# Optimization experiments

Hardware: AMD Instinct MI355X
Metric: run time of the kernel (lower is better)

## Reference

```python
import jax, jax.numpy as jnp
import numpy as np

K = 30  # hardcoded top-k in take_top_k_dropout(x, 30, ...)


def _topk_channel_mask(x, k):
    # x: [B, C, H, W]; binary mask with 1 at the top-k |x| channels per pixel.
    B, C, H, W = x.shape
    xa = jnp.abs(x).reshape(B, C, H * W).transpose(0, 2, 1).reshape(B * H * W, C)
    _, idx = jax.lax.top_k(xa, k)  # [BHW, k]
    rows = jnp.arange(B * H * W)[:, None]
    mask = jnp.zeros((B * H * W, C), x.dtype).at[rows, idx].set(1.0)
    return mask.reshape(B, H * W, C).transpose(0, 2, 1).reshape(B, C, H, W)


def _saturation(z, phi, jump):
    # Saturation_activation_per_filter.forward
    l1 = (jnp.sum(jnp.abs(phi), axis=0) + 1e-12).reshape(1, -1, 1, 1)  # [1,C,1,1]
    r = z / l1
    r = 0.5 * (jnp.sign(r - jump) + jnp.sign(r + jump))
    return r * l1


def _conv_transpose(x, w, b, stride):
    # PyTorch ConvTranspose2d(padding=0): w is [in, out, kh, kw]
    k = w.shape[-1]
    wt = jnp.flip(w, (2, 3)).transpose(1, 0, 2, 3)  # -> [out, in, kh, kw]
    y = jax.lax.conv_general_dilated(
        x, wt, window_strides=(1, 1),
        padding=[(k - 1, k - 1), (k - 1, k - 1)],
        lhs_dilation=(stride, stride),
        dimension_numbers=('NCHW', 'OIHW', 'NCHW'))
    return y + b.reshape(1, -1, 1, 1)


def _take_middle(x):
    width = x.shape[-1]
    s = (width - 32) // 2
    return x[:, :, s:s + 32, s:s + 32]


def setup_inputs() -> dict:
    key = jax.random.key(0)
    ks = jax.random.split(key, 9)
    B, C, H, W, D = 128, 500, 16, 16, 192
    return {
        'x': jax.random.normal(ks[0], (B, C, H, W), jnp.float32),
        'phi': jax.random.normal(ks[1], (D, C), jnp.float32),
        'jump': jnp.float32(0.1),
        'w1': jax.random.normal(ks[2], (C, 300, 4, 4), jnp.float32) * 0.02,
        'b1': jax.random.normal(ks[3], (300,), jnp.float32) * 0.02,
        'w2': jax.random.normal(ks[4], (300, 100, 3, 3), jnp.float32) * 0.02,
        'b2': jax.random.normal(ks[5], (100,), jnp.float32) * 0.02,
        'w3': jax.random.normal(ks[6], (100, 3, 3, 3), jnp.float32) * 0.02,
        'b3': jax.random.normal(ks[7], (3,), jnp.float32) * 0.02,
    }


def reference(x, phi, jump, w1, b1, w2, b2, w3, b3):
    # eval mode: dropout(ones) == ones, no training rescalings
    out = x * _topk_channel_mask(x, K)
    out = _saturation(out, phi, jump)
    out = jax.nn.relu(_conv_transpose(out, w1, b1, 2))
    out = jax.nn.relu(_conv_transpose(out, w2, b2, 1))
    out = jax.nn.relu(_conv_transpose(out, w3, b3, 1))
    return _take_middle(out)
```

## Files before the change

### kernel.cpp

```cpp
#include <hip/hip_runtime.h>
#include <stdint.h>

#define B_   128
#define C_   500
#define H_   16
#define P_   256
#define D_   192
#define C1O  300
#define H1   34
#define P1   (H1*H1)
#define C2O  100
#define H2   36
#define P2   (H2*H2)
#define C3O  3
#define H3   38
#define P3   (H3*H3)
#define CROP 3
#define OW_  32
#define KTOP 30

#define NZQBLK (B_ * 4)
#define NB3BLK ((P3 + 3) / 4)

__device__ __forceinline__ float sgnf(float v){ return (v > 0.f) ? 1.f : ((v < 0.f) ? -1.f : 0.f); }

__device__ __forceinline__ int pat36(int i){
  if (i == 0) return 0;
  if (i == 1) return 1;
  if (i <= 33) return 2;
  if (i == 34) return 3;
  return 4;
}

__global__ void k_setup(const float* __restrict__ phi, const float* __restrict__ jumpp,
                        const float* __restrict__ w2, const float* __restrict__ b1,
                        const float* __restrict__ b2,
                        float* __restrict__ l1, float* __restrict__ thr,
                        float* __restrict__ tab, float4* __restrict__ zero_region){
  const int blk = blockIdx.x;
  const int t = threadIdx.x;

  if (blk >= 101){
    const int idx0 = (blk - 101) * 256 + t;
    const int nvec = (B_ * P1 + B_ * P2) / 16;
    float4 z = make_float4(0.f, 0.f, 0.f, 0.f);
    for (int i = idx0; i < nvec; i += 64 * 256) zero_region[i] = z;
    return;
  }

  if (blk == 100){
    float J = jumpp[0];
    for (int c = t; c < C_; c += 256){
      float s = 0.f;
      for (int d = 0; d < D_; ++d) s += fabsf(phi[d * C_ + c]);
      s += 1e-12f;
      l1[c] = s;
      thr[c] = J * s;
    }
    return;
  }

  __shared__ float S[9];
  if (t < 64){
    const int o = blk;
    float acc[9] = {0,0,0,0,0,0,0,0,0};
    for (int c = t; c < C1O; c += 64){
      float a1 = fmaxf(b1[c], 0.f);
      const float* w = w2 + (c * C2O + o) * 9;
#pragma unroll
      for (int tap = 0; tap < 9; ++tap) acc[tap] += w[tap] * a1;
    }
#pragma unroll
    for (int tap = 0; tap < 9; ++tap)
      for (int off = 32; off; off >>= 1) acc[tap] += __shfl_down(acc[tap], off);
    if (t == 0){
#pragma unroll
      for (int tap = 0; tap < 9; ++tap) S[tap] = acc[tap];
    }
  }
  __syncthreads();
  if (t < 25){
    const int lo[5] = {0,0,0,1,2}, hi[5] = {0,1,2,2,2};
    int pr = t / 5, pc = t % 5;
    float s = b2[blk];
    for (int kh = lo[pr]; kh <= hi[pr]; ++kh)
      for (int kw = lo[pc]; kw <= hi[pc]; ++kw) s += S[kh * 3 + kw];
    tab[blk * 25 + t] = s;
  }
}

__global__ void k_zq_b3(const float* __restrict__ x, const float* __restrict__ l1,
                        const float* __restrict__ thr, const float* __restrict__ jumpp,
                        const float* __restrict__ tab, const float* __restrict__ w3,
                        const float* __restrict__ b3,
                        signed char* __restrict__ zq, unsigned char* __restrict__ d0,
                        float* __restrict__ base3){
  if (blockIdx.x >= NZQBLK){
    const int wave = threadIdx.x >> 6, lane = threadIdx.x & 63;
    const int pix = (blockIdx.x - NZQBLK) * 4 + wave;
    if (pix >= P3) return;
    const int oh = pix / H3, ow = pix % H3;
    float acc[3] = {0, 0, 0};
    for (int c = lane; c < C2O; c += 64){
      const float* w = w3 + c * 27;
#pragma unroll
      for (int kh = 0; kh < 3; ++kh){
        int ih = oh - kh; if (ih < 0 || ih >= H2) continue;
        int prr = pat36(ih) * 5;
#pragma unroll
        for (int kw = 0; kw < 3; ++kw){
          int iw = ow - kw; if (iw < 0 || iw >= H2) continue;
          float a2 = fmaxf(tab[c * 25 + prr + pat36(iw)], 0.f);
#pragma unroll
          for (int o = 0; o < 3; ++o) acc[o] += w[o * 9 + kh * 3 + kw] * a2;
        }
      }
    }
#pragma unroll
    for (int o = 0; o < 3; ++o){
      for (int off = 32; off; off >>= 1) acc[o] += __shfl_down(acc[o], off);
    }
    if (lane == 0){
#pragma unroll
      for (int o = 0; o < 3; ++o) base3[o * P3 + pix] = acc[o] + b3[o];
    }
    return;
  }

  const int b = blockIdx.x >> 2;
  const int tile = (blockIdx.x & 3) * 64;
  const int t = threadIdx.x;
  const int q = t & 15, cg = t >> 4;

  __shared__ unsigned char um[256];
  __shared__ unsigned char pixf[64];
  __shared__ int s_any;
  if (t == 0) s_any = 0;

  unsigned m = 0;
  const int pbase = tile + 4 * q;
  for (int c = cg; c < C_; c += 16){
    float tc = thr[c];
    const float4 v = *(const float4*)(x + ((size_t)(b * C_ + c)) * P_ + pbase);
    if (fabsf(v.x) >= tc) m |= 1u;
    if (fabsf(v.y) >= tc) m |= 2u;
    if (fabsf(v.z) >= tc) m |= 4u;
    if (fabsf(v.w) >= tc) m |= 8u;
  }
  um[t] = (unsigned char)m;
  __syncthreads();
  if (t < 16){
    unsigned mm = 0;
#pragma unroll
    for (int g = 0; g < 16; ++g) mm |= um[g * 16 + t];
#pragma unroll
    for (int j = 0; j < 4; ++j){
      unsigned char f = (unsigned char)((mm >> j) & 1u);
      pixf[4 * t + j] = f;
      d0[b * P_ + tile + 4 * t + j] = f;
    }
    if (mm) s_any = 1;
  }
  __syncthreads();
  if (!s_any) return;

  __shared__ float sx[C_];
  __shared__ unsigned char rm[C_];
  __shared__ unsigned long long red[4];
  __shared__ int sel[KTOP];
  float J = jumpp[0];
  for (int pp = 0; pp < 64; ++pp){
    if (!pixf[pp]) continue;
    int px = tile + pp;
    for (int c = t; c < C_; c += 256){ sx[c] = x[(b * C_ + c) * P_ + px]; rm[c] = 0; }
    __syncthreads();
    for (int it = 0; it < KTOP; ++it){
      unsigned long long best = 0ULL;
      for (int c = t; c < C_; c += 256){
        if (!rm[c]){
          unsigned long long key =
            ((unsigned long long)__float_as_uint(fabsf(sx[c])) << 32) |
            (unsigned int)(C_ - 1 - c);
          if (key > best) best = key;
        }
      }
      for (int off = 32; off; off >>= 1){
        unsigned long long o2 = __shfl_down(best, off);
        if (o2 > best) best = o2;
      }
      if ((t & 63) == 0) red[t >> 6] = best;
      __syncthreads();
      if (t == 0){
        unsigned long long mx = red[0];
        for (int wv = 1; wv < 4; ++wv) if (red[wv] > mx) mx = red[wv];
        int idx = C_ - 1 - (int)(mx & 0xffffffffULL);
        sel[it] = idx;
        rm[idx] = 1;
      }
      __syncthreads();
    }
    for (int c = t; c < C_; c += 256) zq[(b * C_ + c) * P_ + px] = 0;
    __syncthreads();
    if (t < KTOP){
      int c = sel[t];
      float z = sx[c];
      float r = z / l1[c];
      float qv = 0.5f * (sgnf(r - J) + sgnf(r + J));
      int code = (int)(2.f * qv);
      if (code) zq[(b * C_ + c) * P_ + px] = (signed char)code;
    }
    __syncthreads();
  }
}

__global__ void k_u1f(const signed char* __restrict__ zq, const float* __restrict__ l1,
                      const float* __restrict__ w1, const float* __restrict__ b1,
                      const unsigned char* __restrict__ d0,
                      unsigned char* __restrict__ d1, float* __restrict__ u1, int have){
  const int lane = threadIdx.x;
  const int pix0 = blockIdx.x * 64;
  const int tid = pix0 + lane;

  int b = tid / P1, p1 = tid - b * P1;
  int ih = p1 / H1, iw = p1 - ih * H1;
  int h0 = max(0, (ih - 2) >> 1), h1v = min(H_ - 1, ih >> 1);
  int w0 = max(0, (iw - 2) >> 1), w1v = min(H_ - 1, iw >> 1);
  int any = 0;
  for (int h = h0; h <= h1v; ++h)
    for (int w = w0; w <= w1v; ++w)
      any |= d0[b * P_ + h * H_ + w];
  unsigned long long mask = __ballot(any != 0);
  if (!mask) return;
  if (any) d1[tid] = 1;

  while (mask){
    int pp = __ffsll((long long)mask) - 1;
    mask &= mask - 1;
    int pix = pix0 + pp;
    int bb = pix / P1, pq = pix - bb * P1;
    int oih = pq / H1, oiw = pq - oih * H1;
    float acc[5] = {0,0,0,0,0};
    int hh0 = max(0, (oih - 2) >> 1), hh1 = min(H_ - 1, oih >> 1);
    int ww0 = max(0, (oiw - 2) >> 1), ww1 = min(H_ - 1, oiw >> 1);
    for (int h = hh0; h <= hh1; ++h)
      for (int w = ww0; w <= ww1; ++w){
        if (!d0[bb * P_ + h * H_ + w]) continue;
        int kh = oih - 2 * h, kw = oiw - 2 * w;
        const signed char* zp = zq + (size_t)(bb * C_) * P_ + h * H_ + w;
        for (int c = 0; c < C_; ++c){
          int code = zp[(size_t)c * P_];
          if (!code) continue;
          float val = 0.5f * (float)code * l1[c];
          const float* wp = w1 + (size_t)(c * C1O) * 16 + kh * 4 + kw;
#pragma unroll
          for (int j = 0; j < 5; ++j){
            int c1 = j * 64 + lane;
            if (c1 < C1O) acc[j] += wp[(size_t)c1 * 16] * val;
          }
        }
      }
    if (have){
#pragma unroll
      for (int j = 0; j < 5; ++j){
        int c1 = j * 64 + lane;
        if (c1 < C1O){
          float bb1 = b1[c1];
          u1[(size_t)(bb * C1O + c1) * P1 + pq] = fmaxf(bb1 + acc[j], 0.f) - fmaxf(bb1, 0.f);
        }
      }
    }
  }
}

__global__ void k_u2f(const float* __restrict__ u1, const float* __restrict__ w2,
                      const float* __restrict__ tab, const unsigned char* __restrict__ d1,
                      unsigned char* __restrict__ d2, float* __restrict__ u2, int have){
  const int lane = threadIdx.x;
  const int pix0 = blockIdx.x * 64;
  const int tid = pix0 + lane;

  int b = tid / P2, p2 = tid - b * P2;
  int oh = p2 / H2, ow = p2 - oh * H2;
  int any = 0;
  for (int kh = 0; kh < 3; ++kh){
    int ih = oh - kh; if (ih < 0 || ih >= H1) continue;
    for (int kw = 0; kw < 3; ++kw){
      int iw = ow - kw; if (iw < 0 || iw >= H1) continue;
      any |= d1[b * P1 + ih * H1 + iw];
    }
  }
  unsigned long long mask = __ballot(any != 0);
  if (!mask) return;
  if (any) d2[tid] = 1;

  while (mask){
    int pp = __ffsll((long long)mask) - 1;
    mask &= mask - 1;
    int pix = pix0 + pp;
    int bb = pix / P2, pq = pix - bb * P2;
    int ooh = pq / H2, oow = pq - ooh * H2;
    float acc[2] = {0,0};
    for (int kh = 0; kh < 3; ++kh){
      int ih = ooh - kh; if (ih < 0 || ih >= H1) continue;
      for (int kw = 0; kw < 3; ++kw){
        int iw = oow - kw; if (iw < 0 || iw >= H1) continue;
        if (!d1[bb * P1 + ih * H1 + iw]) continue;
        const float* up = u1 + (size_t)(bb * C1O) * P1 + ih * H1 + iw;
        const float* wb = w2 + kh * 3 + kw;
        for (int c1 = 0; c1 < C1O; ++c1){
          float uv = up[(size_t)c1 * P1];
          if (uv == 0.f) continue;
          const float* wp = wb + (size_t)(c1 * C2O) * 9;
#pragma unroll
          for (int j = 0; j < 2; ++j){
            int c2 = j * 64 + lane;
            if (c2 < C2O) acc[j] += wp[(size_t)c2 * 9] * uv;
          }
        }
      }
    }
    if (have){
      int pr = pat36(ooh) * 5 + pat36(oow);
#pragma unroll
      for (int j = 0; j < 2; ++j){
        int c2 = j * 64 + lane;
        if (c2 < C2O){
          float bs = tab[c2 * 25 + pr];
          u2[(size_t)(bb * C2O + c2) * P2 + pq] = fmaxf(bs + acc[j], 0.f) - fmaxf(bs, 0.f);
        }
      }
    }
  }
}

__global__ void k_out(const float* __restrict__ base3, const unsigned char* __restrict__ d2,
                      const float* __restrict__ u2, const float* __restrict__ w3,
                      float* __restrict__ out){
  int tid = blockIdx.x * blockDim.x + threadIdx.x;
  if (tid >= B_ * OW_ * OW_) return;
  int b = tid >> 10;
  int rc = tid & 1023;
  int r = rc >> 5, cc = rc & 31;
  int oh = r + CROP, ow = cc + CROP;
  int any = 0;
#pragma unroll
  for (int kh = 0; kh < 3; ++kh)
#pragma unroll
    for (int kw = 0; kw < 3; ++kw)
      any |= d2[b * P2 + (oh - kh) * H2 + (ow - kw)];
  if (!any){
#pragma unroll
    for (int o = 0; o < 3; ++o)
      out[((b * 3 + o) * OW_ + r) * OW_ + cc] = fmaxf(base3[o * P3 + oh * H3 + ow], 0.f);
    return;
  }
  float acc[3];
#pragma unroll
  for (int o = 0; o < 3; ++o) acc[o] = base3[o * P3 + oh * H3 + ow];
  for (int kh = 0; kh < 3; ++kh){
    int ih = oh - kh;
    for (int kw = 0; kw < 3; ++kw){
      int iw = ow - kw;
      if (!d2[b * P2 + ih * H2 + iw]) continue;
      const float* up = u2 + (size_t)(b * C2O) * P2 + ih * H2 + iw;
      const float* wb = w3 + kh * 3 + kw;
      for (int c2 = 0; c2 < C2O; ++c2){
        float uv = up[(size_t)c2 * P2];
        if (uv == 0.f) continue;
        const float* wp = wb + c2 * 27;
#pragma unroll
        for (int o = 0; o < 3; ++o) acc[o] += wp[o * 9] * uv;
      }
    }
  }
#pragma unroll
  for (int o = 0; o < 3; ++o)
    out[((b * 3 + o) * OW_ + r) * OW_ + cc] = fmaxf(acc[o], 0.f);
}

extern "C" void kernel_launch(void* const* d_in, const int* in_sizes, int n_in,
                              void* d_out, int out_size, void* d_ws, size_t ws_size,
                              hipStream_t stream){
  const float* x   = (const float*)d_in[0];
  const float* phi = (const float*)d_in[1];
  const float* jmp = (const float*)d_in[2];
  const float* w1  = (const float*)d_in[3];
  const float* b1  = (const float*)d_in[4];
  const float* w2  = (const float*)d_in[5];
  const float* b2  = (const float*)d_in[6];
  const float* w3  = (const float*)d_in[7];
  const float* b3  = (const float*)d_in[8];
  float* out = (float*)d_out;
  char* ws = (char*)d_ws;

  constexpr size_t OFF_L1  = 0;
  constexpr size_t OFF_THR = OFF_L1  + 2048;
  constexpr size_t OFF_TAB = OFF_THR + 2048;
  constexpr size_t OFF_B3  = OFF_TAB + 10240;
  constexpr size_t OFF_D0  = OFF_B3  + 17344;
  constexpr size_t OFF_D1  = OFF_D0  + (size_t)B_ * P_;
  constexpr size_t OFF_D2  = OFF_D1  + (size_t)B_ * P1;
  constexpr size_t OFF_ZQ  = OFF_D2  + (size_t)B_ * P2;
  constexpr size_t OFF_U1  = OFF_ZQ  + (size_t)B_ * C_ * P_;
  constexpr size_t OFF_U2  = OFF_U1  + (size_t)B_ * C1O * P1 * 4;
  constexpr size_t TOTAL   = OFF_U2  + (size_t)B_ * C2O * P2 * 4;

  float* l1p  = (float*)(ws + OFF_L1);
  float* thrp = (float*)(ws + OFF_THR);
  float* tabp = (float*)(ws + OFF_TAB);
  float* b3p  = (float*)(ws + OFF_B3);
  unsigned char* d0p = (unsigned char*)(ws + OFF_D0);
  unsigned char* d1p = (unsigned char*)(ws + OFF_D1);
  unsigned char* d2p = (unsigned char*)(ws + OFF_D2);
  signed char* zqp = (signed char*)(ws + OFF_ZQ);
  float* u1p = (float*)(ws + OFF_U1);
  float* u2p = (float*)(ws + OFF_U2);
  int have = (ws_size >= TOTAL) ? 1 : 0;

  k_setup<<<165, 256, 0, stream>>>(phi, jmp, w2, b1, b2, l1p, thrp, tabp, (float4*)d1p);
  k_zq_b3<<<NZQBLK + NB3BLK, 256, 0, stream>>>(x, l1p, thrp, jmp, tabp, w3, b3,
                                               zqp, d0p, b3p);
  k_u1f  <<<(B_ * P1) / 64, 64, 0, stream>>>(zqp, l1p, w1, b1, d0p, d1p, u1p, have);
  k_u2f  <<<(B_ * P2) / 64, 64, 0, stream>>>(u1p, w2, tabp, d1p, d2p, u2p, have);
  k_out  <<<(B_ * OW_ * OW_ + 255) / 256, 256, 0, stream>>>(b3p, d2p, u2p, w3, out);
}
```

Baseline: 144.7 us.

## Add global activity counters to early-exit downstream kernels and parallelize l1 reduction

Adds atomic counters recording whether any tile/wave in each stage is active, so downstream kernels exit immediately when nothing upstream was active. The phi L1 reduction is split across 16 blocks with a shared-memory reduction instead of one block doing all channels serially. k_u1f/k_u2f now use 256-thread blocks with 4 waves, and k_out writes float4 per thread with a fast path for an all-inactive batch. Adds atomics and relies on the threshold structure of the inputs making most work vanish.

New measurement: 132.9 us. -8.2%, faster.

```diff
diff --git a/kernel.cpp b/kernel.cpp
--- a/kernel.cpp
+++ b/kernel.cpp
@@ -19,6 +19,7 @@
 #define OW_  32
 #define KTOP 30
 
+#define NL1B   16
 #define NZQBLK (B_ * 4)
 #define NB3BLK ((P3 + 3) / 4)
 
@@ -40,29 +41,42 @@
   const int blk = blockIdx.x;
   const int t = threadIdx.x;
 
-  if (blk >= 101){
-    const int idx0 = (blk - 101) * 256 + t;
-    const int nvec = (B_ * P1 + B_ * P2) / 16;
+  if (blk >= NL1B + 100){
+    const int idx0 = (blk - (NL1B + 100)) * 256 + t;
+    const int nvec = (16 + B_ * P1 + B_ * P2) / 16;
     float4 z = make_float4(0.f, 0.f, 0.f, 0.f);
     for (int i = idx0; i < nvec; i += 64 * 256) zero_region[i] = z;
     return;
   }
 
-  if (blk == 100){
-    float J = jumpp[0];
-    for (int c = t; c < C_; c += 256){
-      float s = 0.f;
-      for (int d = 0; d < D_; ++d) s += fabsf(phi[d * C_ + c]);
-      s += 1e-12f;
-      l1[c] = s;
-      thr[c] = J * s;
+  if (blk < NL1B){
+    __shared__ float red[8][32];
+    const int cl = t & 31, dg = t >> 5;
+    const int c = blk * 32 + cl;
+    float s = 0.f;
+    if (c < C_){
+      const int d0 = dg * 24;
+#pragma unroll 4
+      for (int d = d0; d < d0 + 24; ++d) s += fabsf(phi[d * C_ + c]);
+    }
+    red[dg][cl] = s;
+    __syncthreads();
+    if (t < 32){
+      int cc = blk * 32 + t;
+      if (cc < C_){
+        float sum = 1e-12f;
+#pragma unroll
+        for (int g = 0; g < 8; ++g) sum += red[g][t];
+        l1[cc] = sum;
+        thr[cc] = jumpp[0] * sum;
+      }
     }
     return;
   }
 
   __shared__ float S[9];
+  const int o = blk - NL1B;
   if (t < 64){
-    const int o = blk;
     float acc[9] = {0,0,0,0,0,0,0,0,0};
     for (int c = t; c < C1O; c += 64){
       float a1 = fmaxf(b1[c], 0.f);
@@ -82,10 +96,10 @@
   if (t < 25){
     const int lo[5] = {0,0,0,1,2}, hi[5] = {0,1,2,2,2};
     int pr = t / 5, pc = t % 5;
-    float s = b2[blk];
+    float s = b2[o];
     for (int kh = lo[pr]; kh <= hi[pr]; ++kh)
       for (int kw = lo[pc]; kw <= hi[pc]; ++kw) s += S[kh * 3 + kw];
-    tab[blk * 25 + t] = s;
+    tab[o * 25 + t] = s;
   }
 }
 
@@ -94,7 +108,7 @@
                         const float* __restrict__ tab, const float* __restrict__ w3,
                         const float* __restrict__ b3,
                         signed char* __restrict__ zq, unsigned char* __restrict__ d0,
-                        float* __restrict__ base3){
+                        float* __restrict__ base3, int* __restrict__ cnt){
   if (blockIdx.x >= NZQBLK){
     const int wave = threadIdx.x >> 6, lane = threadIdx.x & 63;
     const int pix = (blockIdx.x - NZQBLK) * 4 + wave;
@@ -162,6 +176,7 @@
     if (mm) s_any = 1;
   }
   __syncthreads();
+  if (t == 0 && s_any) atomicAdd(cnt, 1);
   if (!s_any) return;
 
   __shared__ float sx[C_];
@@ -215,10 +230,12 @@
 
 __global__ void k_u1f(const signed char* __restrict__ zq, const float* __restrict__ l1,
                       const float* __restrict__ w1, const float* __restrict__ b1,
-                      const unsigned char* __restrict__ d0,
+                      const unsigned char* __restrict__ d0, const int* __restrict__ cnt,
+                      int* __restrict__ cnt1,
                       unsigned char* __restrict__ d1, float* __restrict__ u1, int have){
-  const int lane = threadIdx.x;
-  const int pix0 = blockIdx.x * 64;
+  if (cnt[0] == 0) return;
+  const int wave = threadIdx.x >> 6, lane = threadIdx.x & 63;
+  const int pix0 = (blockIdx.x * 4 + wave) * 64;
   const int tid = pix0 + lane;
 
   int b = tid / P1, p1 = tid - b * P1;
@@ -232,6 +249,7 @@
   unsigned long long mask = __ballot(any != 0);
   if (!mask) return;
   if (any) d1[tid] = 1;
+  if (lane == 0) atomicAdd(cnt1, 1);
 
   while (mask){
     int pp = __ffsll((long long)mask) - 1;
@@ -274,9 +292,11 @@
 
 __global__ void k_u2f(const float* __restrict__ u1, const float* __restrict__ w2,
                       const float* __restrict__ tab, const unsigned char* __restrict__ d1,
+                      const int* __restrict__ cnt1, int* __restrict__ cnt2,
                       unsigned char* __restrict__ d2, float* __restrict__ u2, int have){
-  const int lane = threadIdx.x;
-  const int pix0 = blockIdx.x * 64;
+  if (cnt1[0] == 0) return;
+  const int wave = threadIdx.x >> 6, lane = threadIdx.x & 63;
+  const int pix0 = (blockIdx.x * 4 + wave) * 64;
   const int tid = pix0 + lane;
 
   int b = tid / P2, p2 = tid - b * P2;
@@ -292,6 +312,7 @@
   unsigned long long mask = __ballot(any != 0);
   if (!mask) return;
   if (any) d2[tid] = 1;
+  if (lane == 0) atomicAdd(cnt2, 1);
 
   while (mask){
     int pp = __ffsll((long long)mask) - 1;
@@ -335,47 +356,46 @@
 
 __global__ void k_out(const float* __restrict__ base3, const unsigned char* __restrict__ d2,
                       const float* __restrict__ u2, const float* __restrict__ w3,
-                      float* __restrict__ out){
+                      const int* __restrict__ cnt2, float* __restrict__ out){
   int tid = blockIdx.x * blockDim.x + threadIdx.x;
-  if (tid >= B_ * OW_ * OW_) return;
-  int b = tid >> 10;
-  int rc = tid & 1023;
-  int r = rc >> 5, cc = rc & 31;
-  int oh = r + CROP, ow = cc + CROP;
-  int any = 0;
-#pragma unroll
-  for (int kh = 0; kh < 3; ++kh)
-#pragma unroll
-    for (int kw = 0; kw < 3; ++kw)
-      any |= d2[b * P2 + (oh - kh) * H2 + (ow - kw)];
-  if (!any){
-#pragma unroll
-    for (int o = 0; o < 3; ++o)
-      out[((b * 3 + o) * OW_ + r) * OW_ + cc] = fmaxf(base3[o * P3 + oh * H3 + ow], 0.f);
-    return;
-  }
-  float acc[3];
-#pragma unroll
-  for (int o = 0; o < 3; ++o) acc[o] = base3[o * P3 + oh * H3 + ow];
-  for (int kh = 0; kh < 3; ++kh){
-    int ih = oh - kh;
-    for (int kw = 0; kw < 3; ++kw){
-      int iw = ow - kw;
-      if (!d2[b * P2 + ih * H2 + iw]) continue;
-      const float* up = u2 + (size_t)(b * C2O) * P2 + ih * H2 + iw;
-      const float* wb = w3 + kh * 3 + kw;
-      for (int c2 = 0; c2 < C2O; ++c2){
-        float uv = up[(size_t)c2 * P2];
-        if (uv == 0.f) continue;
-        const float* wp = wb + c2 * 27;
-#pragma unroll
-        for (int o = 0; o < 3; ++o) acc[o] += wp[o * 9] * uv;
-      }
-    }
-  }
-#pragma unroll
-  for (int o = 0; o < 3; ++o)
-    out[((b * 3 + o) * OW_ + r) * OW_ + cc] = fmaxf(acc[o], 0.f);
+  if (tid >= B_ * 3 * OW_ * (OW_ / 4)) return;
+  const int perimg = 3 * OW_ * (OW_ / 4);
+  int b = tid / perimg;
+  int rem = tid - b * perimg;
+  int o = rem >> 8;
+  int rr = rem & 255;
+  int r = rr >> 3, q4 = rr & 7;
+  int oh = r + CROP;
+  int ow0 = q4 * 4 + CROP;
+  const float* bp = base3 + o * P3 + oh * H3 + ow0;
+
+  float4 res;
+  float* rp = &res.x;
+  if (cnt2[0] == 0){
+#pragma unroll
+    for (int j = 0; j < 4; ++j) rp[j] = fmaxf(bp[j], 0.f);
+  } else {
+#pragma unroll
+    for (int j = 0; j < 4; ++j){
+      int ow = ow0 + j;
+      float acc = bp[j];
+      for (int kh = 0; kh < 3; ++kh){
+        int ih = oh - kh;
+        for (int kw = 0; kw < 3; ++kw){
+          int iw = ow - kw;
+          if (!d2[b * P2 + ih * H2 + iw]) continue;
+          const float* up = u2 + (size_t)(b * C2O) * P2 + ih * H2 + iw;
+          const float* wp = w3 + o * 9 + kh * 3 + kw;
+          for (int c2 = 0; c2 < C2O; ++c2){
+            float uv = up[(size_t)c2 * P2];
+            if (uv != 0.f) acc += wp[c2 * 27] * uv;
+          }
+        }
+      }
+      rp[j] = fmaxf(acc, 0.f);
+    }
+  }
+  *(float4*)(out + ((size_t)(b * 3 + o) * OW_ + r) * OW_ + q4 * 4) = res;
 }
 
 extern "C" void kernel_launch(void* const* d_in, const int* in_sizes, int n_in,
@@ -398,7 +418,8 @@
   constexpr size_t OFF_TAB = OFF_THR + 2048;
   constexpr size_t OFF_B3  = OFF_TAB + 10240;
   constexpr size_t OFF_D0  = OFF_B3  + 17344;
-  constexpr size_t OFF_D1  = OFF_D0  + (size_t)B_ * P_;
+  constexpr size_t OFF_CNT = OFF_D0  + (size_t)B_ * P_;
+  constexpr size_t OFF_D1  = OFF_CNT + 16;
   constexpr size_t OFF_D2  = OFF_D1  + (size_t)B_ * P1;
   constexpr size_t OFF_ZQ  = OFF_D2  + (size_t)B_ * P2;
   constexpr size_t OFF_U1  = OFF_ZQ  + (size_t)B_ * C_ * P_;
@@ -410,6 +431,7 @@
   float* tabp = (float*)(ws + OFF_TAB);
   float* b3p  = (float*)(ws + OFF_B3);
   unsigned char* d0p = (unsigned char*)(ws + OFF_D0);
+  int* cntp = (int*)(ws + OFF_CNT);
   unsigned char* d1p = (unsigned char*)(ws + OFF_D1);
   unsigned char* d2p = (unsigned char*)(ws + OFF_D2);
   signed char* zqp = (signed char*)(ws + OFF_ZQ);
@@ -417,10 +439,14 @@
   float* u2p = (float*)(ws + OFF_U2);
   int have = (ws_size >= TOTAL) ? 1 : 0;
 
-  k_setup<<<165, 256, 0, stream>>>(phi, jmp, w2, b1, b2, l1p, thrp, tabp, (float4*)d1p);
+  k_setup<<<NL1B + 100 + 64, 256, 0, stream>>>(phi, jmp, w2, b1, b2,
+                                               l1p, thrp, tabp, (float4*)cntp);
   k_zq_b3<<<NZQBLK + NB3BLK, 256, 0, stream>>>(x, l1p, thrp, jmp, tabp, w3, b3,
-                                               zqp, d0p, b3p);
-  k_u1f  <<<(B_ * P1) / 64, 64, 0, stream>>>(zqp, l1p, w1, b1, d0p, d1p, u1p, have);
-  k_u2f  <<<(B_ * P2) / 64, 64, 0, stream>>>(u1p, w2, tabp, d1p, d2p, u2p, have);
-  k_out  <<<(B_ * OW_ * OW_ + 255) / 256, 256, 0, stream>>>(b3p, d2p, u2p, w3, out);
-}
+                                               zqp, d0p, b3p, cntp);
+  k_u1f  <<<(B_ * P1) / 256, 256, 0, stream>>>(zqp, l1p, w1, b1, d0p, cntp, cntp + 1,
+                                               d1p, u1p, have);
+  k_u2f  <<<(B_ * P2) / 256, 256, 0, stream>>>(u1p, w2, tabp, d1p, cntp + 1, cntp + 2,
+                                               d2p, u2p, have);
+  k_out  <<<(B_ * 3 * OW_ * (OW_ / 4) + 255) / 256, 256, 0, stream>>>(
+      b3p, d2p, u2p, w3, cntp + 2, out);
+}
```
